# Optimization experiments

Measured on AMD Instinct MI355X. Metric: run time of the kernel, lower is better.

## Reference

```python
import jax, jax.numpy as jnp
import numpy as np

# --- constants from the module (KANLayer passes degree=3; BSplineActivation defaults) ---
K = 5          # num_control_points
DEG = 3        # degree
G = 3          # grid points (set_grid_points(3) in __init__)
LO, HI = -1.0, 1.0  # grid_range


def basis_table():
    """Precompute the shared [G, K] normalized Gaussian basis table (same for all edges)."""
    knots = np.linspace(LO - DEG * 0.1, HI + DEG * 0.1, K + DEG + 1)
    grid = np.linspace(LO, HI, G)
    bv = np.zeros((G, K), dtype=np.float32)
    for i in range(K):
        center = (knots[i + DEG // 2] + knots[i + DEG // 2 + 1]) / 2.0
        width = (knots[i + DEG + 1] - knots[i]) / 2.0
        bv[:, i] = np.exp(-(((grid - center) / width) ** 2))
    bv = bv / (bv.sum(axis=1, keepdims=True) + 1e-6)
    return jnp.asarray(bv)


def kan_layer(x, cp, bw, sw, imp, bv):
    """Fused KANLayer: x [B,I]; cp [I,J,K]; bw/sw/imp [I,J]; bv [G,K] -> [B,J]."""
    xc = jnp.clip(x, LO, HI)
    gi = (xc - LO) / (HI - LO) * (G - 1)                     # [B,I] in [0, G-1]
    lo = jnp.clip(jnp.floor(gi).astype(jnp.int32), 0, G - 1)
    hi = jnp.clip(jnp.ceil(gi).astype(jnp.int32), 0, G - 1)
    frac = (gi - lo.astype(gi.dtype))[..., None]             # [B,I,1]
    basis = bv[lo] * (1.0 - frac) + bv[hi] * frac            # [B,I,K] gather + lerp
    base = x * jax.nn.sigmoid(x)                             # SiLU base function, [B,I]
    # out[b,j] = sum_i imp[i,j] * (bw[i,j]*base[b,i] + sw[i,j]*basis[b,i,:]@cp[i,j,:])
    out = jnp.einsum('bi,ij->bj', base, imp * bw)
    out = out + jnp.einsum('bik,ijk->bj', basis, imp[:, :, None] * sw[:, :, None] * cp)
    return out


def setup_inputs() -> dict:
    key = jax.random.key(0)
    ks = jax.random.split(key, 9)
    B, D0, D1, D2 = 131072, 64, 128, 64
    return {
        'x': jax.random.normal(ks[0], (B, D0), dtype=jnp.float32),
        'cp0': jax.random.normal(ks[1], (D0, D1, K), dtype=jnp.float32) * 0.1,
        'bw0': jax.random.normal(ks[2], (D0, D1), dtype=jnp.float32),
        'sw0': jax.random.normal(ks[3], (D0, D1), dtype=jnp.float32),
        'imp0': jnp.ones((D0, D1), dtype=jnp.float32),
        'cp1': jax.random.normal(ks[4], (D1, D2, K), dtype=jnp.float32) * 0.1,
        'bw1': jax.random.normal(ks[5], (D1, D2), dtype=jnp.float32),
        'sw1': jax.random.normal(ks[6], (D1, D2), dtype=jnp.float32),
        'imp1': jnp.ones((D1, D2), dtype=jnp.float32),
    }


def reference(x, cp0, bw0, sw0, imp0, cp1, bw1, sw1, imp1):
    bv = basis_table()
    h = kan_layer(x, cp0, bw0, sw0, imp0, bv)
    return kan_layer(h, cp1, bw1, sw1, imp1, bv)
```

## Files before the change

### kernel.cpp

```cpp
#include <hip/hip_runtime.h>
#include <math.h>

typedef __attribute__((ext_vector_type(8))) _Float16 f16x8;
typedef __attribute__((ext_vector_type(2))) _Float16 f16x2;
typedef __attribute__((ext_vector_type(4))) float f32x4;


#define TPB 512
#define BM  256
#define HSTRIDE 272
#define LDS_TOT (BM * HSTRIDE)

__global__ __launch_bounds__(TPB, 2) void kan_mfma_kernel(
    const float* __restrict__ x, const _Float16* __restrict__ W0t,
    const _Float16* __restrict__ W1t, const float* __restrict__ bias0,
    const float* __restrict__ bias1, float* __restrict__ out)
{
    __shared__ char smem[LDS_TOT];
    const int tid  = threadIdx.x;
    const int lane = tid & 63;
    const int wid  = tid >> 6;
    const int gq   = lane >> 4;
    const int lm   = lane & 15;
    const int wavebase = wid * 32;
    const long rowbase = (long)blockIdx.x * BM;

#if __has_builtin(__builtin_amdgcn_cvt_pkrtz)
    auto pk2 = [](float a, float b) -> f16x2 {
        return (f16x2)__builtin_amdgcn_cvt_pkrtz(a, b);
    };
#else
    auto pk2 = [](float a, float b) -> f16x2 {
        return f16x2{(_Float16)a, (_Float16)b};
    };
#endif
#if __has_builtin(__builtin_amdgcn_rcpf)
    auto frcp = [](float a) -> float { return __builtin_amdgcn_rcpf(a); };
#else
    auto frcp = [](float a) -> float { return 1.0f / a; };
#endif

    auto buildFeats4 = [&](const float* v, f16x8* dst) {
        union U { f16x8 v8; f16x2 h2[4]; } u0, u1, u2, u3;
        #pragma unroll
        for (int q = 0; q < 4; ++q) {
            float va = v[2 * q], vb = v[2 * q + 1];
            float ba = va * frcp(1.0f + __expf(-va));
            float bb = vb * frcp(1.0f + __expf(-vb));
            float ga = fminf(fmaxf(va, -1.f), 1.f) + 1.f;
            float gb = fminf(fmaxf(vb, -1.f), 1.f) + 1.f;
            float s1a = (ga >= 1.f) ? 1.f : 0.f;
            float s1b = (gb >= 1.f) ? 1.f : 0.f;
            float sga = (ga >= 1.f) ? ga : 0.f;
            float sgb = (gb >= 1.f) ? gb : 0.f;
            u0.h2[q] = pk2(ba, bb);
            u1.h2[q] = pk2(ga, gb);
            u2.h2[q] = pk2(s1a, s1b);
            u3.h2[q] = pk2(sga, sgb);
        }
        dst[0] = u0.v8; dst[1] = u1.v8; dst[2] = u2.v8; dst[3] = u3.v8;
    };

    float b0v[8], b1v[4];
    #pragma unroll
    for (int nf = 0; nf < 8; ++nf) b0v[nf] = bias0[nf * 16 + lm];
    #pragma unroll
    for (int nf = 0; nf < 4; ++nf) b1v[nf] = bias1[nf * 16 + lm];

    float v0[2][8], v1[2][8];
    #pragma unroll
    for (int mi = 0; mi < 2; ++mi) {
        const float* xp = x + (rowbase + wavebase + mi * 16 + lm) * 64 + gq * 8;
        float4 a0 = *(const float4*)(xp);
        float4 a1 = *(const float4*)(xp + 4);
        float4 a2 = *(const float4*)(xp + 32);
        float4 a3 = *(const float4*)(xp + 36);
        v0[mi][0]=a0.x; v0[mi][1]=a0.y; v0[mi][2]=a0.z; v0[mi][3]=a0.w;
        v0[mi][4]=a1.x; v0[mi][5]=a1.y; v0[mi][6]=a1.z; v0[mi][7]=a1.w;
        v1[mi][0]=a2.x; v1[mi][1]=a2.y; v1[mi][2]=a2.z; v1[mi][3]=a2.w;
        v1[mi][4]=a3.x; v1[mi][5]=a3.y; v1[mi][6]=a3.z; v1[mi][7]=a3.w;
    }

    f32x4 acc[2][8] = {};
    {
        const char* w0 = (const char*)W0t + gq * 2048 + lm * 16;
        f16x8 b0[8], b1[8];
        #pragma unroll
        for (int nf = 0; nf < 8; ++nf) b0[nf] = *(const f16x8*)(w0 + nf * 256);

        f16x8 fr[2][4];
        buildFeats4(v0[0], fr[0]);
        buildFeats4(v0[1], fr[1]);

#define L0_STEP(S, C, CUR, NXT) do {                                          \
        if ((S) < 7) {                                                        \
            _Pragma("unroll")                                                 \
            for (int nf = 0; nf < 8; ++nf)                                    \
                NXT[nf] = *(const f16x8*)(w0 + ((S) + 1) * 8192 + nf * 256);  \
        }                                                                     \
        _Pragma("unroll")                                                     \
        for (int mi = 0; mi < 2; ++mi) {                                      \
            f16x8 a = fr[mi][C];                                              \
            _Pragma("unroll")                                                 \
            for (int nf = 0; nf < 8; ++nf)                                    \
                acc[mi][nf] = __builtin_amdgcn_mfma_f32_16x16x32_f16(         \
                    a, CUR[nf], acc[mi][nf], 0, 0, 0);                        \
        }                                                                     \
    } while (0)

        L0_STEP(0, 0, b0, b1); L0_STEP(1, 1, b1, b0);
        L0_STEP(2, 2, b0, b1); L0_STEP(3, 3, b1, b0);
        buildFeats4(v1[0], fr[0]);
        buildFeats4(v1[1], fr[1]);
        L0_STEP(4, 0, b0, b1); L0_STEP(5, 1, b1, b0);
        L0_STEP(6, 2, b0, b1); L0_STEP(7, 3, b1, b0);
#undef L0_STEP
    }

    #pragma unroll
    for (int mi = 0; mi < 2; ++mi)
        #pragma unroll
        for (int nf = 0; nf < 8; ++nf)
            #pragma unroll
            for (int rg = 0; rg < 4; ++rg)
                *(_Float16*)(smem + (wavebase + mi * 16 + gq * 4 + rg) * HSTRIDE
                             + (nf * 16 + lm) * 2) = (_Float16)(acc[mi][nf][rg] + b0v[nf]);
    __syncthreads();

    f32x4 accO[2][4] = {};
    #pragma unroll
    for (int half = 0; half < 2; ++half) {
        float hv0[2][8], hv1[2][8];
        #pragma unroll
        for (int mi = 0; mi < 2; ++mi) {
            const char* hrow = smem + (wavebase + mi * 16 + lm) * HSTRIDE;
            f16x8 ha = *(const f16x8*)(hrow + (half * 64 + gq * 8) * 2);
            f16x8 hb = *(const f16x8*)(hrow + (half * 64 + 32 + gq * 8) * 2);
            #pragma unroll
            for (int e = 0; e < 8; ++e) { hv0[mi][e] = (float)ha[e]; hv1[mi][e] = (float)hb[e]; }
        }

        const char* w1 = (const char*)W1t + half * 32768 + gq * 1024 + lm * 16;
        f16x8 c0[4], c1[4];
        #pragma unroll
        for (int nf = 0; nf < 4; ++nf) c0[nf] = *(const f16x8*)(w1 + nf * 256);

        f16x8 fr[2][4];
        buildFeats4(hv0[0], fr[0]);
        buildFeats4(hv0[1], fr[1]);

#define L1_STEP(S, C, CUR, NXT) do {                                          \
        if ((S) < 7) {                                                        \
            _Pragma("unroll")                                                 \
            for (int nf = 0; nf < 4; ++nf)                                    \
                NXT[nf] = *(const f16x8*)(w1 + ((S) + 1) * 4096 + nf * 256);  \
        }                                                                     \
        _Pragma("unroll")                                                     \
        for (int mi = 0; mi < 2; ++mi) {                                      \
            f16x8 a = fr[mi][C];                                              \
            _Pragma("unroll")                                                 \
            for (int nf = 0; nf < 4; ++nf)                                    \
                accO[mi][nf] = __builtin_amdgcn_mfma_f32_16x16x32_f16(        \
                    a, CUR[nf], accO[mi][nf], 0, 0, 0);                       \
        }                                                                     \
    } while (0)

        L1_STEP(0, 0, c0, c1); L1_STEP(1, 1, c1, c0);
        L1_STEP(2, 2, c0, c1); L1_STEP(3, 3, c1, c0);
        buildFeats4(hv1[0], fr[0]);
        buildFeats4(hv1[1], fr[1]);
        L1_STEP(4, 0, c0, c1); L1_STEP(5, 1, c1, c0);
        L1_STEP(6, 2, c0, c1); L1_STEP(7, 3, c1, c0);
#undef L1_STEP
    }

    float* og = out + (rowbase + wavebase) * 64;
    #pragma unroll
    for (int mi = 0; mi < 2; ++mi)
        #pragma unroll
        for (int nf = 0; nf < 4; ++nf)
            #pragma unroll
            for (int rg = 0; rg < 4; ++rg)
                og[(mi * 16 + gq * 4 + rg) * 64 + nf * 16 + lm] = accO[mi][nf][rg] + b1v[nf];
}

__global__ __launch_bounds__(256) void kan_combine_w(
    const float* __restrict__ cp0, const float* __restrict__ bw0,
    const float* __restrict__ sw0, const float* __restrict__ imp0,
    const float* __restrict__ cp1, const float* __restrict__ bw1,
    const float* __restrict__ sw1, const float* __restrict__ imp1,
    _Float16* __restrict__ W0t, _Float16* __restrict__ W1t,
    float* __restrict__ bias0, float* __restrict__ bias1)
{
    float bvv[3][5];
    #pragma unroll
    for (int g = 0; g < 3; ++g) {
        float gv = (float)g - 1.0f;
        float e[5]; float s = 0.f;
        #pragma unroll
        for (int i = 0; i < 5; ++i) {
            float cc = -0.8125f + 0.325f * (float)i;
            float d  = (gv - cc) * (1.0f / 0.65f);
            e[i] = __expf(-d * d); s += e[i];
        }
        float inv = 1.0f / (s + 1e-6f);
        #pragma unroll
        for (int i = 0; i < 5; ++i) bvv[g][i] = e[i] * inv;
    }

    auto wval = [&](const float* cp, float bw, float sw, float imp, int q) -> float {
        if (q == 0) return imp * bw;
        float P0 = 0.f, Q0 = 0.f, P1 = 0.f, Q1 = 0.f;
        #pragma unroll
        for (int c = 0; c < 5; ++c) {
            P0 += cp[c] * bvv[0][c];
            Q0 += cp[c] * (bvv[1][c] - bvv[0][c]);
            P1 += cp[c] * (2.f * bvv[1][c] - bvv[2][c]);
            Q1 += cp[c] * (bvv[2][c] - bvv[1][c]);
        }
        float r = (q == 1) ? Q0 : (q == 2) ? (P1 - P0) : (Q1 - Q0);
        return imp * sw * r;
    };
    auto p0val = [&](const float* cp) -> float {
        float P0 = 0.f;
        #pragma unroll
        for (int c = 0; c < 5; ++c) P0 += cp[c] * bvv[0][c];
        return P0;
    };

    const int bx = blockIdx.x;
    const int t  = threadIdx.x;

    if (bx < 256) {
        int f = bx * 256 + t;
        if (f < 32768) {
            int e = f & 7, n = (f >> 3) & 127, g = (f >> 10) & 3, s = f >> 12;
            int ih = s >> 2, q = s & 3;
            int i = ih * 32 + g * 8 + e;
            int edge = i * 128 + n;
            W0t[f] = (_Float16)wval(cp0 + edge * 5, bw0[edge], sw0[edge], imp0[edge], q);
        } else {
            int f2 = f - 32768;
            int e = f2 & 7, n = (f2 >> 3) & 63, g = (f2 >> 9) & 3;
            int tq = f2 >> 11;
            int half = tq >> 3, s = tq & 7;
            int ih = s >> 2, q = s & 3;
            int i2 = half * 64 + ih * 32 + g * 8 + e;
            int edge = i2 * 64 + n;
            W1t[f2] = (_Float16)wval(cp1 + edge * 5, bw1[edge], sw1[edge], imp1[edge], q);
        }
    } else if (bx == 256) {
        __shared__ float part[256];
        int j = t >> 1, h = t & 1;
        float s = 0.f;
        #pragma unroll 4
        for (int i = h * 32; i < h * 32 + 32; ++i) {
            int edge = i * 128 + j;
            s += imp0[edge] * sw0[edge] * p0val(cp0 + edge * 5);
        }
        part[t] = s;
        __syncthreads();
        if (t < 128) bias0[t] = part[2 * t] + part[2 * t + 1];
    } else {
        __shared__ float part[256];
        int j = t >> 2, qtr = t & 3;
        float s = 0.f;
        #pragma unroll 4
        for (int i2 = qtr * 32; i2 < qtr * 32 + 32; ++i2) {
            int edge = i2 * 64 + j;
            s += imp1[edge] * sw1[edge] * p0val(cp1 + edge * 5);
        }
        part[t] = s;
        __syncthreads();
        if (t < 64) bias1[t] = part[4 * t] + part[4 * t + 1] + part[4 * t + 2] + part[4 * t + 3];
    }
}

#define NTHR 256
#define JT 32
#define WS8 8

#define STAGE_L0(JBASE) do {                                                  \
    _Pragma("unroll")                                                         \
    for (int p = 0; p < 8; ++p) {                                             \
        int idx = tid + p * NTHR;                                             \
        int i  = idx >> 5;                                                    \
        int jj = idx & 31;                                                    \
        int e  = i * 128 + (JBASE) + jj;                                      \
        float im = imp0[e];                                                   \
        float wb = bw0[e] * im;                                               \
        float ws = sw0[e] * im;                                               \
        const float* cp = cp0 + e * 5;                                        \
        float* wp = wbuf + idx * WS8;                                         \
        wp[0] = wb;                                                           \
        wp[1] = ws * cp[0]; wp[2] = ws * cp[1]; wp[3] = ws * cp[2];           \
        wp[4] = ws * cp[3]; wp[5] = ws * cp[4];                               \
    }                                                                         \
} while (0)

#define STAGE_L1(IBASE, JBASE) do {                                           \
    _Pragma("unroll")                                                         \
    for (int p = 0; p < 8; ++p) {                                             \
        int idx = tid + p * NTHR;                                             \
        int ii = idx >> 5;                                                    \
        int jj = idx & 31;                                                    \
        int e  = ((IBASE) + ii) * 64 + (JBASE) + jj;                          \
        float im = imp1[e];                                                   \
        float wb = bw1[e] * im;                                               \
        float ws = sw1[e] * im;                                               \
        const float* cp = cp1 + e * 5;                                        \
        float* wp = wbuf + idx * WS8;                                         \
        wp[0] = wb;                                                           \
        wp[1] = ws * cp[0]; wp[2] = ws * cp[1]; wp[3] = ws * cp[2];           \
        wp[4] = ws * cp[3]; wp[5] = ws * cp[4];                               \
    }                                                                         \
} while (0)

#define COMPUTE_TILE(ACC) do {                                                \
    _Pragma("unroll 2")                                                       \
    for (int i = 0; i < 64; ++i) {                                            \
        float v  = vbuf[i][tid];                                              \
        float sg = 1.0f / (1.0f + __expf(-v));                                \
        float base = v * sg;                                                  \
        float xc = fminf(fmaxf(v, -1.0f), 1.0f);                              \
        float gi = xc + 1.0f;                                                 \
        int lo = (int)gi; lo = (lo > 2) ? 2 : lo;                             \
        float fr = gi - (float)lo;                                            \
        int hi = (fr > 0.0f) ? (lo + 1) : lo;                                 \
        float b0 = bvt[lo][0]; b0 += (bvt[hi][0] - b0) * fr;                  \
        float b1 = bvt[lo][1]; b1 += (bvt[hi][1] - b1) * fr;                  \
        float b2 = bvt[lo][2]; b2 += (bvt[hi][2] - b2) * fr;                  \
        float b3 = bvt[lo][3]; b3 += (bvt[hi][3] - b3) * fr;                  \
        float b4 = bvt[lo][4]; b4 += (bvt[hi][4] - b4) * fr;                  \
        const float* wr = wbuf + i * (JT * WS8);                              \
        _Pragma("unroll")                                                     \
        for (int jj = 0; jj < JT; ++jj) {                                     \
            const float* wp = wr + jj * WS8;                                  \
            float a = ACC[jj];                                                \
            a = fmaf(wp[0], base, a);                                         \
            a = fmaf(wp[1], b0, a);                                           \
            a = fmaf(wp[2], b1, a);                                           \
            a = fmaf(wp[3], b2, a);                                           \
            a = fmaf(wp[4], b3, a);                                           \
            a = fmaf(wp[5], b4, a);                                           \
            ACC[jj] = a;                                                      \
        }                                                                     \
    }                                                                         \
} while (0)

__global__ __launch_bounds__(NTHR) void kan_fused_kernel(
    const float* __restrict__ x,
    const float* __restrict__ cp0, const float* __restrict__ bw0,
    const float* __restrict__ sw0, const float* __restrict__ imp0,
    const float* __restrict__ cp1, const float* __restrict__ bw1,
    const float* __restrict__ sw1, const float* __restrict__ imp1,
    float* __restrict__ out)
{
    __shared__ float vbuf[64][NTHR + 1];
    __shared__ float wbuf[64 * JT * WS8];
    __shared__ float bvt[3][8];

    const int tid = threadIdx.x;

    if (tid < 3) {
        float gv = -1.0f + (float)tid;
        float e[5];
        float s = 0.0f;
        #pragma unroll
        for (int i = 0; i < 5; ++i) {
            float c = -0.8125f + 0.325f * (float)i;
            float d = (gv - c) * (1.0f / 0.65f);
            e[i] = expf(-d * d);
            s += e[i];
        }
        float inv = 1.0f / (s + 1e-6f);
        #pragma unroll
        for (int i = 0; i < 5; ++i) bvt[tid][i] = e[i] * inv;
    }

    {
        const float4* xg = (const float4*)(x + (size_t)blockIdx.x * (NTHR * 64));
        #pragma unroll
        for (int it = 0; it < 16; ++it) {
            int e4 = tid + it * NTHR;
            float4 v = xg[e4];
            int r  = e4 >> 4;
            int ib = (e4 & 15) << 2;
            vbuf[ib + 0][r] = v.x;
            vbuf[ib + 1][r] = v.y;
            vbuf[ib + 2][r] = v.z;
            vbuf[ib + 3][r] = v.w;
        }
    }
    __syncthreads();

    float h0[32] = {}, h1[32] = {}, h2[32] = {}, h3[32] = {};
    STAGE_L0(0);   __syncthreads(); COMPUTE_TILE(h0); __syncthreads();
    STAGE_L0(32);  __syncthreads(); COMPUTE_TILE(h1); __syncthreads();
    STAGE_L0(64);  __syncthreads(); COMPUTE_TILE(h2); __syncthreads();
    STAGE_L0(96);  __syncthreads(); COMPUTE_TILE(h3); __syncthreads();

    #pragma unroll
    for (int i = 0; i < 32; ++i) vbuf[i][tid] = h0[i];
    #pragma unroll
    for (int i = 0; i < 32; ++i) vbuf[32 + i][tid] = h1[i];

    float o0[32] = {}, o1[32] = {};
    STAGE_L1(0, 0);   __syncthreads(); COMPUTE_TILE(o0); __syncthreads();
    STAGE_L1(0, 32);  __syncthreads(); COMPUTE_TILE(o1); __syncthreads();

    #pragma unroll
    for (int i = 0; i < 32; ++i) vbuf[i][tid] = h2[i];
    #pragma unroll
    for (int i = 0; i < 32; ++i) vbuf[32 + i][tid] = h3[i];

    STAGE_L1(64, 0);  __syncthreads(); COMPUTE_TILE(o0); __syncthreads();
    STAGE_L1(64, 32); __syncthreads(); COMPUTE_TILE(o1);

    float4* og = (float4*)(out + (size_t)blockIdx.x * (NTHR * 64) + (size_t)tid * 64);
    #pragma unroll
    for (int q = 0; q < 8; ++q)
        og[q] = make_float4(o0[4 * q + 0], o0[4 * q + 1], o0[4 * q + 2], o0[4 * q + 3]);
    #pragma unroll
    for (int q = 0; q < 8; ++q)
        og[8 + q] = make_float4(o1[4 * q + 0], o1[4 * q + 1], o1[4 * q + 2], o1[4 * q + 3]);
}

extern "C" void kernel_launch(void* const* d_in, const int* in_sizes, int n_in,
                              void* d_out, int out_size, void* d_ws, size_t ws_size,
                              hipStream_t stream) {
    const float* x    = (const float*)d_in[0];
    const float* cp0  = (const float*)d_in[1];
    const float* bw0  = (const float*)d_in[2];
    const float* sw0  = (const float*)d_in[3];
    const float* imp0 = (const float*)d_in[4];
    const float* cp1  = (const float*)d_in[5];
    const float* bw1  = (const float*)d_in[6];
    const float* sw1  = (const float*)d_in[7];
    const float* imp1 = (const float*)d_in[8];
    float* out = (float*)d_out;

    const int B = in_sizes[0] / 64;
    const size_t need = 65536 * sizeof(_Float16) + 192 * sizeof(float);

    if (ws_size >= need && (B % BM) == 0) {
        _Float16* W0t = (_Float16*)d_ws;
        _Float16* W1t = W0t + 32768;
        float* bias0 = (float*)(W1t + 32768);
        float* bias1 = bias0 + 128;
        kan_combine_w<<<258, 256, 0, stream>>>(cp0, bw0, sw0, imp0,
                                               cp1, bw1, sw1, imp1,
                                               W0t, W1t, bias0, bias1);
        kan_mfma_kernel<<<B / BM, TPB, 0, stream>>>(x, W0t, W1t, bias0, bias1, out);
    } else {
        kan_fused_kernel<<<B / NTHR, NTHR, 0, stream>>>(
            x, cp0, bw0, sw0, imp0, cp1, bw1, sw1, imp1, out);
    }
}
```

Before: 44.23 us.

## Give each wave 64 rows, halve threads per block, and XOR-swizzle the LDS hidden tile

Each block now runs 4 waves instead of 8, and each wave processes 64 rows (4 M-fragments) instead of 32. Every weight fragment loaded from global memory is therefore reused across 4 MFMAs rather than 2, which halves the weight-load traffic per row. The padded LDS stride for the hidden activations is replaced by a dense 256-byte stride with an XOR swizzle to avoid bank conflicts. In exchange, register pressure roughly doubles for the accumulators, and the explicit double-buffered weight prefetch is dropped in favour of per-step loads. Together these risk spills or lower occupancy.

```diff
diff --git a/kernel.cpp b/kernel.cpp
--- a/kernel.cpp
+++ b/kernel.cpp
@@ -6,10 +6,9 @@
 typedef __attribute__((ext_vector_type(4))) float f32x4;
 
 
-#define TPB 512
+#define TPB 256
 #define BM  256
-#define HSTRIDE 272
-#define LDS_TOT (BM * HSTRIDE)
+#define LDS_TOT 65536
 
 __global__ __launch_bounds__(TPB, 2) void kan_mfma_kernel(
     const float* __restrict__ x, const _Float16* __restrict__ W0t,
@@ -22,7 +21,7 @@
     const int wid  = tid >> 6;
     const int gq   = lane >> 4;
     const int lm   = lane & 15;
-    const int wavebase = wid * 32;
+    const int wavebase = wid * 64;
     const long rowbase = (long)blockIdx.x * BM;
 
 #if __has_builtin(__builtin_amdgcn_cvt_pkrtz)
@@ -61,127 +60,104 @@
         dst[0] = u0.v8; dst[1] = u1.v8; dst[2] = u2.v8; dst[3] = u3.v8;
     };
 
-    float b0v[8], b1v[4];
-    #pragma unroll
-    for (int nf = 0; nf < 8; ++nf) b0v[nf] = bias0[nf * 16 + lm];
-    #pragma unroll
-    for (int nf = 0; nf < 4; ++nf) b1v[nf] = bias1[nf * 16 + lm];
-
-    float v0[2][8], v1[2][8];
-    #pragma unroll
-    for (int mi = 0; mi < 2; ++mi) {
-        const float* xp = x + (rowbase + wavebase + mi * 16 + lm) * 64 + gq * 8;
+    auto buildFromX = [&](int mi, int ih, f16x8* dst) {
+        const float* xp = x + (rowbase + wavebase + mi * 16 + lm) * 64
+                          + ih * 32 + gq * 8;
         float4 a0 = *(const float4*)(xp);
         float4 a1 = *(const float4*)(xp + 4);
-        float4 a2 = *(const float4*)(xp + 32);
-        float4 a3 = *(const float4*)(xp + 36);
-        v0[mi][0]=a0.x; v0[mi][1]=a0.y; v0[mi][2]=a0.z; v0[mi][3]=a0.w;
-        v0[mi][4]=a1.x; v0[mi][5]=a1.y; v0[mi][6]=a1.z; v0[mi][7]=a1.w;
-        v1[mi][0]=a2.x; v1[mi][1]=a2.y; v1[mi][2]=a2.z; v1[mi][3]=a2.w;
-        v1[mi][4]=a3.x; v1[mi][5]=a3.y; v1[mi][6]=a3.z; v1[mi][7]=a3.w;
-    }
-
-    f32x4 acc[2][8] = {};
+        float v[8] = {a0.x, a0.y, a0.z, a0.w, a1.x, a1.y, a1.z, a1.w};
+        buildFeats4(v, dst);
+    };
+
+    float b0v[8], b1v[4];
+    #pragma unroll
+    for (int nf = 0; nf < 8; ++nf) b0v[nf] = bias0[nf * 16 + lm];
+    #pragma unroll
+    for (int nf = 0; nf < 4; ++nf) b1v[nf] = bias1[nf * 16 + lm];
+
+    f32x4 acc[4][8] = {};
+    f16x8 fr[4][4];
     {
         const char* w0 = (const char*)W0t + gq * 2048 + lm * 16;
-        f16x8 b0[8], b1[8];
-        #pragma unroll
-        for (int nf = 0; nf < 8; ++nf) b0[nf] = *(const f16x8*)(w0 + nf * 256);
-
-        f16x8 fr[2][4];
-        buildFeats4(v0[0], fr[0]);
-        buildFeats4(v0[1], fr[1]);
-
-#define L0_STEP(S, C, CUR, NXT) do {                                          \
-        if ((S) < 7) {                                                        \
+        #pragma unroll
+        for (int mi = 0; mi < 4; ++mi) buildFromX(mi, 0, fr[mi]);
+
+#define L0_STEP(S, C) do {                                                    \
+        _Pragma("unroll")                                                     \
+        for (int nf = 0; nf < 8; ++nf) {                                      \
+            f16x8 b = *(const f16x8*)(w0 + (S) * 8192 + nf * 256);            \
             _Pragma("unroll")                                                 \
-            for (int nf = 0; nf < 8; ++nf)                                    \
-                NXT[nf] = *(const f16x8*)(w0 + ((S) + 1) * 8192 + nf * 256);  \
-        }                                                                     \
-        _Pragma("unroll")                                                     \
-        for (int mi = 0; mi < 2; ++mi) {                                      \
-            f16x8 a = fr[mi][C];                                              \
-            _Pragma("unroll")                                                 \
-            for (int nf = 0; nf < 8; ++nf)                                    \
+            for (int mi = 0; mi < 4; ++mi)                                    \
                 acc[mi][nf] = __builtin_amdgcn_mfma_f32_16x16x32_f16(         \
-                    a, CUR[nf], acc[mi][nf], 0, 0, 0);                        \
+                    fr[mi][C], b, acc[mi][nf], 0, 0, 0);                      \
         }                                                                     \
     } while (0)
 
-        L0_STEP(0, 0, b0, b1); L0_STEP(1, 1, b1, b0);
-        L0_STEP(2, 2, b0, b1); L0_STEP(3, 3, b1, b0);
-        buildFeats4(v1[0], fr[0]);
-        buildFeats4(v1[1], fr[1]);
-        L0_STEP(4, 0, b0, b1); L0_STEP(5, 1, b1, b0);
-        L0_STEP(6, 2, b0, b1); L0_STEP(7, 3, b1, b0);
+        L0_STEP(0, 0); L0_STEP(1, 1); L0_STEP(2, 2); L0_STEP(3, 3);
+        #pragma unroll
+        for (int mi = 0; mi < 4; ++mi) buildFromX(mi, 1, fr[mi]);
+        L0_STEP(4, 0); L0_STEP(5, 1); L0_STEP(6, 2); L0_STEP(7, 3);
 #undef L0_STEP
     }
 
     #pragma unroll
-    for (int mi = 0; mi < 2; ++mi)
+    for (int mi = 0; mi < 4; ++mi)
         #pragma unroll
         for (int nf = 0; nf < 8; ++nf)
             #pragma unroll
-            for (int rg = 0; rg < 4; ++rg)
-                *(_Float16*)(smem + (wavebase + mi * 16 + gq * 4 + rg) * HSTRIDE
-                             + (nf * 16 + lm) * 2) = (_Float16)(acc[mi][nf][rg] + b0v[nf]);
+            for (int rg = 0; rg < 4; ++rg) {
+                int row  = wavebase + mi * 16 + gq * 4 + rg;
+                int byte = (row * 256 + (nf * 16 + lm) * 2) ^ ((row & 7) << 4);
+                *(_Float16*)(smem + byte) = (_Float16)(acc[mi][nf][rg] + b0v[nf]);
+            }
     __syncthreads();
 
-    f32x4 accO[2][4] = {};
-    #pragma unroll
-    for (int half = 0; half < 2; ++half) {
-        float hv0[2][8], hv1[2][8];
-        #pragma unroll
-        for (int mi = 0; mi < 2; ++mi) {
-            const char* hrow = smem + (wavebase + mi * 16 + lm) * HSTRIDE;
-            f16x8 ha = *(const f16x8*)(hrow + (half * 64 + gq * 8) * 2);
-            f16x8 hb = *(const f16x8*)(hrow + (half * 64 + 32 + gq * 8) * 2);
+    f32x4 accO[4][4] = {};
+    #pragma unroll
+    for (int i2h = 0; i2h < 2; ++i2h) {
+        const char* w1 = (const char*)W1t + i2h * 32768 + gq * 1024 + lm * 16;
+
+        auto buildFromH = [&](int mi, int ih, f16x8* dst) {
+            int row  = wavebase + mi * 16 + lm;
+            int byte = (row * 256 + (i2h * 64 + ih * 32 + gq * 8) * 2)
+                       ^ ((row & 7) << 4);
+            f16x8 hv = *(const f16x8*)(smem + byte);
+            float v[8];
             #pragma unroll
-            for (int e = 0; e < 8; ++e) { hv0[mi][e] = (float)ha[e]; hv1[mi][e] = (float)hb[e]; }
-        }
-
-        const char* w1 = (const char*)W1t + half * 32768 + gq * 1024 + lm * 16;
-        f16x8 c0[4], c1[4];
-        #pragma unroll
-        for (int nf = 0; nf < 4; ++nf) c0[nf] = *(const f16x8*)(w1 + nf * 256);
-
-        f16x8 fr[2][4];
-        buildFeats4(hv0[0], fr[0]);
-        buildFeats4(hv0[1], fr[1]);
-
-#define L1_STEP(S, C, CUR, NXT) do {                                          \
-        if ((S) < 7) {                                                        \
+            for (int e = 0; e < 8; ++e) v[e] = (float)hv[e];
+            buildFeats4(v, dst);
+        };
+
+        #pragma unroll
+        for (int mi = 0; mi < 4; ++mi) buildFromH(mi, 0, fr[mi]);
+
+#define L1_STEP(S, C) do {                                                    \
+        _Pragma("unroll")                                                     \
+        for (int nf = 0; nf < 4; ++nf) {                                      \
+            f16x8 c = *(const f16x8*)(w1 + (S) * 4096 + nf * 256);            \
             _Pragma("unroll")                                                 \
-            for (int nf = 0; nf < 4; ++nf)                                    \
-                NXT[nf] = *(const f16x8*)(w1 + ((S) + 1) * 4096 + nf * 256);  \
-        }                                                                     \
-        _Pragma("unroll")                                                     \
-        for (int mi = 0; mi < 2; ++mi) {                                      \
-            f16x8 a = fr[mi][C];                                              \
-            _Pragma("unroll")                                                 \
-            for (int nf = 0; nf < 4; ++nf)                                    \
+            for (int mi = 0; mi < 4; ++mi)                                    \
                 accO[mi][nf] = __builtin_amdgcn_mfma_f32_16x16x32_f16(        \
-                    a, CUR[nf], accO[mi][nf], 0, 0, 0);                       \
+                    fr[mi][C], c, accO[mi][nf], 0, 0, 0);                     \
         }                                                                     \
     } while (0)
 
-        L1_STEP(0, 0, c0, c1); L1_STEP(1, 1, c1, c0);
-        L1_STEP(2, 2, c0, c1); L1_STEP(3, 3, c1, c0);
-        buildFeats4(hv1[0], fr[0]);
-        buildFeats4(hv1[1], fr[1]);
-        L1_STEP(4, 0, c0, c1); L1_STEP(5, 1, c1, c0);
-        L1_STEP(6, 2, c0, c1); L1_STEP(7, 3, c1, c0);
+        L1_STEP(0, 0); L1_STEP(1, 1); L1_STEP(2, 2); L1_STEP(3, 3);
+        #pragma unroll
+        for (int mi = 0; mi < 4; ++mi) buildFromH(mi, 1, fr[mi]);
+        L1_STEP(4, 0); L1_STEP(5, 1); L1_STEP(6, 2); L1_STEP(7, 3);
 #undef L1_STEP
     }
 
     float* og = out + (rowbase + wavebase) * 64;
     #pragma unroll
-    for (int mi = 0; mi < 2; ++mi)
+    for (int mi = 0; mi < 4; ++mi)
         #pragma unroll
         for (int nf = 0; nf < 4; ++nf)
             #pragma unroll
             for (int rg = 0; rg < 4; ++rg)
-                og[(mi * 16 + gq * 4 + rg) * 64 + nf * 16 + lm] = accO[mi][nf][rg] + b1v[nf];
+                og[(mi * 16 + gq * 4 + rg) * 64 + nf * 16 + lm]
+                    = accO[mi][nf][rg] + b1v[nf];
 }
 
 __global__ __launch_bounds__(256) void kan_combine_w(
```

Measured after the change: 42.15 us. 1.05x faster.
